# Performance work log

Hardware: AMD Instinct MI355X
Metric: run time of the kernel (lower is better)

## Reference

```python
import jax, jax.numpy as jnp
import numpy as np

B, T, C = 2, 2048, 1024
H = 16
HD = C // H  # head_size = 64
FF = 2 * C   # ffwd_size default = n_embd * 2
EPS = float(jnp.finfo(jnp.float32).eps)  # torch RMSNorm eps=None -> finfo eps


def rmsnorm(x, g):
    # torch.nn.RMSNorm: x / sqrt(mean(x^2) + eps) * weight
    ms = jnp.mean(jnp.square(x), axis=-1, keepdims=True)
    return x * jax.lax.rsqrt(ms + EPS) * g


def setup_inputs() -> dict:
    key = jax.random.key(0)
    ks = jax.random.split(key, 12)
    s_in = 1.0 / np.sqrt(C)
    s_ff = 1.0 / np.sqrt(FF)
    return {
        "target": jax.random.normal(ks[0], (B, T, C), dtype=jnp.float32),
        # per-head projections, torch Linear layout [out, in] stacked over heads: [H, HD, C]
        "wq": jax.random.uniform(ks[1], (H, HD, C), jnp.float32, -s_in, s_in),
        "wk": jax.random.uniform(ks[2], (H, HD, C), jnp.float32, -s_in, s_in),
        "wv": jax.random.uniform(ks[3], (H, HD, C), jnp.float32, -s_in, s_in),
        "w_proj": jax.random.uniform(ks[4], (C, H * HD), jnp.float32, -s_in, s_in),
        "b_proj": jax.random.uniform(ks[5], (C,), jnp.float32, -s_in, s_in),
        "w1": jax.random.uniform(ks[6], (FF, C), jnp.float32, -s_in, s_in),
        "b1": jax.random.uniform(ks[7], (FF,), jnp.float32, -s_in, s_in),
        "w2": jax.random.uniform(ks[8], (C, FF), jnp.float32, -s_ff, s_ff),
        "b2": jax.random.uniform(ks[9], (C,), jnp.float32, -s_ff, s_ff),
        "g1": jnp.ones((C,), jnp.float32),
        "g2": jnp.ones((C,), jnp.float32),
    }


def reference(target, wq, wk, wv, w_proj, b_proj, w1, b1, w2, b2, g1, g2):
    x = rmsnorm(target, g1)
    # q,k,v: [B,H,T,HD]
    q = jnp.einsum("btc,hdc->bhtd", x, wq)
    k = jnp.einsum("btc,hdc->bhtd", x, wk)
    v = jnp.einsum("btc,hdc->bhtd", x, wv)
    scale = HD ** -0.5
    wei = jnp.einsum("bhtd,bhsd->bhts", q, k) * scale  # [B,H,T,T]
    causal = jnp.tril(jnp.ones((T, T), dtype=bool))
    wei = jnp.where(causal, wei, -jnp.inf)
    wei = jax.nn.softmax(wei, axis=-1)
    attn = jnp.einsum("bhts,bhsd->bhtd", wei, v)  # [B,H,T,HD]
    attn = attn.transpose(0, 2, 1, 3).reshape(B, T, H * HD)  # concat heads
    attn = attn @ w_proj.T + b_proj
    target = target + attn
    y = rmsnorm(target, g2)
    h = jax.nn.gelu(y @ w1.T + b1, approximate=False)  # torch nn.GELU default = exact
    ff = h @ w2.T + b2
    return target + ff
```

## Files before the change

### kernel.cpp

```cpp
#include <hip/hip_runtime.h>
#include <math.h>

#define B_  2
#define T_  2048
#define C_  1024
#define H_  16
#define HD_ 64
#define FF_ 2048
#define EPS_ 1.1920929e-07f

typedef __attribute__((ext_vector_type(8))) short short8;
typedef __attribute__((ext_vector_type(4))) float f32x4;

__device__ __forceinline__ unsigned short f2bf(float f) {
    unsigned u = __float_as_uint(f);
    u += 0x7fffu + ((u >> 16) & 1u);
    return (unsigned short)(u >> 16);
}
__device__ __forceinline__ float bf2f(unsigned short u) {
    return __uint_as_float(((unsigned)u) << 16);
}

__global__ void convert_weights(const float* __restrict__ wq, const float* __restrict__ wk,
                                const float* __restrict__ wv, const float* __restrict__ wp,
                                const float* __restrict__ w1, const float* __restrict__ w2,
                                unsigned short* __restrict__ dst) {
    size_t i = ((size_t)blockIdx.x * 256 + threadIdx.x) * 4;
    const float* src; size_t off = i;
    if      (i < 1048576u)  { src = wq; }
    else if (i < 2097152u)  { src = wk; off = i - 1048576u; }
    else if (i < 3145728u)  { src = wv; off = i - 2097152u; }
    else if (i < 4194304u)  { src = wp; off = i - 3145728u; }
    else if (i < 6291456u)  { src = w1; off = i - 4194304u; }
    else                    { src = w2; off = i - 6291456u; }
    float4 v4 = *(const float4*)(src + off);
    ushort4 o4;
    o4.x = f2bf(v4.x); o4.y = f2bf(v4.y); o4.z = f2bf(v4.z); o4.w = f2bf(v4.w);
    *(ushort4*)(dst + i) = o4;
}

__global__ void rmsnorm_bf16_kernel(const float* __restrict__ x, const float* __restrict__ g,
                                    unsigned short* __restrict__ y) {
    int row = blockIdx.x;
    int tid = threadIdx.x;
    const float4* xr = (const float4*)(x + (size_t)row * C_);
    float4 xv = xr[tid];
    float ss = xv.x * xv.x + xv.y * xv.y + xv.z * xv.z + xv.w * xv.w;
    #pragma unroll
    for (int m = 32; m >= 1; m >>= 1) ss += __shfl_xor(ss, m, 64);
    __shared__ float sred[4];
    if ((tid & 63) == 0) sred[tid >> 6] = ss;
    __syncthreads();
    float tot = sred[0] + sred[1] + sred[2] + sred[3];
    float r = rsqrtf(tot * (1.0f / C_) + EPS_);
    float4 gv = ((const float4*)g)[tid];
    ushort4 o;
    o.x = f2bf(xv.x * r * gv.x);
    o.y = f2bf(xv.y * r * gv.y);
    o.z = f2bf(xv.z * r * gv.z);
    o.w = f2bf(xv.w * r * gv.w);
    *((ushort4*)(y + (size_t)row * C_) + tid) = o;
}

template <int ACT, bool BIAS, bool RES, bool OBF16, bool QKV>
__global__ __launch_bounds__(256) void mfma_gemm(
        const unsigned short* __restrict__ A,
        const unsigned short* __restrict__ W0, const unsigned short* __restrict__ W1,
        const unsigned short* __restrict__ W2,
        const float* __restrict__ bias, const float* __restrict__ resid,
        void* __restrict__ O0, void* __restrict__ O1, void* __restrict__ O2,
        int M, int N, int K) {
    __shared__ short As[128 * 32];
    __shared__ short Bs[128 * 32];
    const int tid  = threadIdx.x;
    const int w    = tid >> 6, lane = tid & 63;
    const int tileN = blockIdx.x * 128, tileM = blockIdx.y * 128;

    const unsigned short* Wp = W0;
    void* Op = O0;
    if (QKV) {
        int z = blockIdx.z;
        if (z == 1) { Wp = W1; Op = O1; }
        else if (z == 2) { Wp = W2; Op = O2; }
    }

    const int c0 = 2 * w, c1 = 2 * w + 1;
    const unsigned short* ga0 = A  + (size_t)(tileM + c0 * 16 + (lane >> 2)) * K + (lane & 3) * 8;
    const unsigned short* ga1 = A  + (size_t)(tileM + c1 * 16 + (lane >> 2)) * K + (lane & 3) * 8;
    const unsigned short* gb0 = Wp + (size_t)(tileN + c0 * 16 + (lane >> 2)) * K + (lane & 3) * 8;
    const unsigned short* gb1 = Wp + (size_t)(tileN + c1 * 16 + (lane >> 2)) * K + (lane & 3) * 8;

    f32x4 acc[4][4];
    const f32x4 zed = {0.f, 0.f, 0.f, 0.f};
    #pragma unroll
    for (int i = 0; i < 4; ++i)
        #pragma unroll
        for (int j = 0; j < 4; ++j) acc[i][j] = zed;

    const int wm = (w >> 1) * 64, wn = (w & 1) * 64;
    const int frow = lane & 15, koff = (lane >> 4) * 8;

    for (int k0 = 0; k0 < K; k0 += 32) {
        __builtin_amdgcn_global_load_lds(
            (const __attribute__((address_space(1))) unsigned*)(ga0 + k0),
            (__attribute__((address_space(3))) unsigned*)(As + c0 * 512), 16, 0, 0);
        __builtin_amdgcn_global_load_lds(
            (const __attribute__((address_space(1))) unsigned*)(ga1 + k0),
            (__attribute__((address_space(3))) unsigned*)(As + c1 * 512), 16, 0, 0);
        __builtin_amdgcn_global_load_lds(
            (const __attribute__((address_space(1))) unsigned*)(gb0 + k0),
            (__attribute__((address_space(3))) unsigned*)(Bs + c0 * 512), 16, 0, 0);
        __builtin_amdgcn_global_load_lds(
            (const __attribute__((address_space(1))) unsigned*)(gb1 + k0),
            (__attribute__((address_space(3))) unsigned*)(Bs + c1 * 512), 16, 0, 0);
        __syncthreads();

        short8 af[4], bfr[4];
        #pragma unroll
        for (int i = 0; i < 4; ++i)
            af[i] = *(const short8*)(As + (wm + i * 16 + frow) * 32 + koff);
        #pragma unroll
        for (int j = 0; j < 4; ++j)
            bfr[j] = *(const short8*)(Bs + (wn + j * 16 + frow) * 32 + koff);
        #pragma unroll
        for (int i = 0; i < 4; ++i)
            #pragma unroll
            for (int j = 0; j < 4; ++j)
                acc[i][j] = __builtin_amdgcn_mfma_f32_16x16x32_bf16(af[i], bfr[j], acc[i][j], 0, 0, 0);
        __syncthreads();
    }

    const int ecol = lane & 15, erow = (lane >> 4) * 4;
    const bool isQ  = QKV && (blockIdx.z == 0);
    const bool isVT = QKV && (blockIdx.z == 2);
    #pragma unroll
    for (int j = 0; j < 4; ++j) {
        int n = tileN + wn + j * 16 + ecol;
        float bv = BIAS ? bias[n] : 0.f;
        #pragma unroll
        for (int i = 0; i < 4; ++i) {
            int mbase = tileM + wm + i * 16 + erow;
            #pragma unroll
            for (int r = 0; r < 4; ++r) {
                float val = acc[i][j][r] + bv;
                if (ACT == 1) val = 0.5f * val * (1.0f + erff(val * 0.70710678118654752f));
                int mrow = mbase + r;
                if (isQ) val *= 0.125f;
                if (isVT) {
                    int bb = mrow >> 11, tt = mrow & 2047;
                    int hh = n >> 6, dd = n & 63;
                    size_t idx = ((size_t)((bb * 16 + hh) * 64 + dd)) * 2048 + tt;
                    ((unsigned short*)Op)[idx] = f2bf(val);
                } else {
                    size_t idx = (size_t)mrow * N + n;
                    if (RES) val += resid[idx];
                    if (OBF16) ((unsigned short*)Op)[idx] = f2bf(val);
                    else       ((float*)Op)[idx] = val;
                }
            }
        }
    }
}

__global__ __launch_bounds__(256) void flash_mfma_kernel(
        const unsigned short* __restrict__ q, const unsigned short* __restrict__ k,
        const unsigned short* __restrict__ vT, unsigned short* __restrict__ out) {
    __shared__ unsigned short Ks[64 * 72];
    __shared__ unsigned short Vt[64 * 72];
    __shared__ unsigned short Ps[4 * 16 * 40];

    const int tid  = threadIdx.x;
    const int w    = tid >> 6, lane = tid & 63;
    const int quad = lane >> 4, l15 = lane & 15;
    const int bh = blockIdx.x;
    const int qt = (gridDim.y - 1) - blockIdx.y;
    const int h = bh & (H_ - 1);
    const int b = bh >> 4;

    const size_t qkbase = (size_t)b * T_ * C_ + h * HD_;
    const size_t vbase  = (size_t)(b * H_ + h) * HD_ * T_;

    short8 QB[2];
    {
        const unsigned short* qp = q + qkbase + (size_t)(qt * 64 + w * 16 + l15) * C_;
        QB[0] = *(const short8*)(qp + quad * 8);
        QB[1] = *(const short8*)(qp + 32 + quad * 8);
    }

    f32x4 O[4];
    const f32x4 zed = {0.f, 0.f, 0.f, 0.f};
    #pragma unroll
    for (int dt = 0; dt < 4; ++dt) O[dt] = zed;
    float m_i = -INFINITY, l_i = 0.f;

    const int qg = qt * 64 + w * 16 + l15;
    const int psoff = w * 640 + l15 * 40;
    const int sr = tid >> 3, sp = tid & 7;

    for (int st = 0; st <= qt; ++st) {
        const int s0 = st * 64;
        {
            const unsigned short* kp = k + qkbase + (size_t)(s0 + sr) * C_ + sp * 8;
            *(short8*)&Ks[sr * 72 + sp * 8]        = *(const short8*)kp;
            *(short8*)&Ks[(sr + 32) * 72 + sp * 8] = *(const short8*)(kp + 32 * C_);
            const unsigned short* vp = vT + vbase + (size_t)sr * T_ + s0 + sp * 8;
            *(short8*)&Vt[sr * 72 + sp * 8]        = *(const short8*)vp;
            *(short8*)&Vt[(sr + 32) * 72 + sp * 8] = *(const short8*)(vp + 32 * T_);
        }
        __syncthreads();

        const bool diag = (st == qt);
        #pragma unroll
        for (int sb = 0; sb < 2; ++sb) {
            const int sbl = sb * 32;
            f32x4 Sacc[2];
            #pragma unroll
            for (int u = 0; u < 2; ++u) {
                const unsigned short* kr = &Ks[(sbl + 16 * u + l15) * 72 + quad * 8];
                short8 KA0 = *(const short8*)kr;
                short8 KA1 = *(const short8*)(kr + 32);
                Sacc[u] = __builtin_amdgcn_mfma_f32_16x16x32_bf16(KA0, QB[0], zed, 0, 0, 0);
                Sacc[u] = __builtin_amdgcn_mfma_f32_16x16x32_bf16(KA1, QB[1], Sacc[u], 0, 0, 0);
            }
            float vals[8];
            #pragma unroll
            for (int u = 0; u < 2; ++u)
                #pragma unroll
                for (int r = 0; r < 4; ++r) vals[u * 4 + r] = Sacc[u][r];
            if (diag) {
                #pragma unroll
                for (int u = 0; u < 2; ++u)
                    #pragma unroll
                    for (int r = 0; r < 4; ++r) {
                        int sg = s0 + sbl + 16 * u + quad * 4 + r;
                        if (sg > qg) vals[u * 4 + r] = -INFINITY;
                    }
            }
            float mx = vals[0];
            #pragma unroll
            for (int i = 1; i < 8; ++i) mx = fmaxf(mx, vals[i]);
            mx = fmaxf(mx, __shfl_xor(mx, 16, 64));
            mx = fmaxf(mx, __shfl_xor(mx, 32, 64));
            float mnew = fmaxf(m_i, mx);
            float alpha = __expf(m_i - mnew);
            m_i = mnew;
            float rs = 0.f;
            #pragma unroll
            for (int i = 0; i < 8; ++i) { vals[i] = __expf(vals[i] - mnew); rs += vals[i]; }
            rs += __shfl_xor(rs, 16, 64);
            rs += __shfl_xor(rs, 32, 64);
            l_i = l_i * alpha + rs;

            #pragma unroll
            for (int u = 0; u < 2; ++u) {
                uint2 pw;
                pw.x = (unsigned)f2bf(vals[u * 4 + 0]) | ((unsigned)f2bf(vals[u * 4 + 1]) << 16);
                pw.y = (unsigned)f2bf(vals[u * 4 + 2]) | ((unsigned)f2bf(vals[u * 4 + 3]) << 16);
                *(uint2*)&Ps[psoff + 16 * u + quad * 4] = pw;
            }
            __syncthreads();

            f32x4 av;
            #pragma unroll
            for (int r = 0; r < 4; ++r) av[r] = __shfl(alpha, quad * 4 + r, 64);
            #pragma unroll
            for (int dt = 0; dt < 4; ++dt)
                #pragma unroll
                for (int r = 0; r < 4; ++r) O[dt][r] *= av[r];
            short8 PA = *(const short8*)&Ps[psoff + quad * 8];
            #pragma unroll
            for (int dt = 0; dt < 4; ++dt) {
                short8 VB = *(const short8*)&Vt[(16 * dt + l15) * 72 + sbl + quad * 8];
                O[dt] = __builtin_amdgcn_mfma_f32_16x16x32_bf16(PA, VB, O[dt], 0, 0, 0);
            }
            __syncthreads();
        }
    }

    f32x4 inv;
    #pragma unroll
    for (int r = 0; r < 4; ++r) inv[r] = 1.0f / __shfl(l_i, quad * 4 + r, 64);
    #pragma unroll
    for (int dt = 0; dt < 4; ++dt)
        #pragma unroll
        for (int r = 0; r < 4; ++r) {
            int row = qt * 64 + w * 16 + quad * 4 + r;
            int col = h * HD_ + dt * 16 + l15;
            out[((size_t)(b * T_ + row)) * C_ + col] = f2bf(O[dt][r] * inv[r]);
        }
}

extern "C" void kernel_launch(void* const* d_in, const int* in_sizes, int n_in,
                              void* d_out, int out_size, void* d_ws, size_t ws_size,
                              hipStream_t stream) {
    const float* target = (const float*)d_in[0];
    const float* wq     = (const float*)d_in[1];
    const float* wk     = (const float*)d_in[2];
    const float* wv     = (const float*)d_in[3];
    const float* w_proj = (const float*)d_in[4];
    const float* b_proj = (const float*)d_in[5];
    const float* w1     = (const float*)d_in[6];
    const float* b1     = (const float*)d_in[7];
    const float* w2     = (const float*)d_in[8];
    const float* b2     = (const float*)d_in[9];
    const float* g1     = (const float*)d_in[10];
    const float* g2     = (const float*)d_in[11];
    float* out = (float*)d_out;

    char* ws = (char*)d_ws;
    const size_t MB = 1u << 20;
    unsigned short* xn = (unsigned short*)(ws);
    unsigned short* q  = (unsigned short*)(ws + 8 * MB);
    unsigned short* k  = (unsigned short*)(ws + 16 * MB);
    unsigned short* vt = (unsigned short*)(ws + 24 * MB);
    float*          x2 = (float*)(ws + 32 * MB);
    unsigned short* wb = (unsigned short*)(ws + 48 * MB);
    unsigned short* y  = q;
    unsigned short* hb = k;

    unsigned short* wq_b = wb;
    unsigned short* wk_b = wb + 1048576u;
    unsigned short* wv_b = wb + 2097152u;
    unsigned short* wp_b = wb + 3145728u;
    unsigned short* w1_b = wb + 4194304u;
    unsigned short* w2_b = wb + 6291456u;

    const int M = B_ * T_;

    convert_weights<<<8192, 256, 0, stream>>>(wq, wk, wv, w_proj, w1, w2, wb);
    rmsnorm_bf16_kernel<<<M, 256, 0, stream>>>(target, g1, xn);

    mfma_gemm<0, false, false, true, true><<<dim3(C_ / 128, M / 128, 3), 256, 0, stream>>>(
        xn, wq_b, wk_b, wv_b, nullptr, nullptr, q, k, vt, M, C_, C_);

    flash_mfma_kernel<<<dim3(B_ * H_, T_ / 64), 256, 0, stream>>>(q, k, vt, xn);

    mfma_gemm<0, true, true, false, false><<<dim3(C_ / 128, M / 128, 1), 256, 0, stream>>>(
        xn, wp_b, wp_b, wp_b, b_proj, target, x2, x2, x2, M, C_, C_);

    rmsnorm_bf16_kernel<<<M, 256, 0, stream>>>(x2, g2, y);

    mfma_gemm<1, true, false, true, false><<<dim3(FF_ / 128, M / 128, 1), 256, 0, stream>>>(
        y, w1_b, w1_b, w1_b, b1, nullptr, hb, hb, hb, M, FF_, C_);

    mfma_gemm<0, true, true, false, false><<<dim3(C_ / 128, M / 128, 1), 256, 0, stream>>>(
        hb, w2_b, w2_b, w2_b, b2, x2, out, out, out, M, C_, FF_);
}
```

Before: 338.8 us.

## Templatize GEMM M-tile, fuse QKV into one wide GEMM, double-buffer flash P

The GEMM takes the M tile height as a template parameter and spreads its global-to-LDS chunk loads across warps generically. The proj, FF1 and FF2 GEMMs now use 64-row tiles, which doubles the number of blocks on this large-CU GPU at the cost of less reuse per block. QKV runs as a single N=3072 GEMM that sends each output column to q, k or transposed v by its column range, relying on the three weight matrices sitting next to each other. In the flash kernel the P buffer is double-buffered by sub-block, so the barrier after the PV MFMA moves out of the inner loop, removing one sync per inner iteration at the cost of extra LDS.

```diff
diff --git a/kernel.cpp b/kernel.cpp
--- a/kernel.cpp
+++ b/kernel.cpp
@@ -62,68 +62,63 @@
     *((ushort4*)(y + (size_t)row * C_) + tid) = o;
 }
 
-template <int ACT, bool BIAS, bool RES, bool OBF16, bool QKV>
+template <int TM, int ACT, bool BIAS, bool RES, bool OBF16, int ROUTE>
 __global__ __launch_bounds__(256) void mfma_gemm(
-        const unsigned short* __restrict__ A,
-        const unsigned short* __restrict__ W0, const unsigned short* __restrict__ W1,
-        const unsigned short* __restrict__ W2,
+        const unsigned short* __restrict__ A, const unsigned short* __restrict__ W,
         const float* __restrict__ bias, const float* __restrict__ resid,
         void* __restrict__ O0, void* __restrict__ O1, void* __restrict__ O2,
         int M, int N, int K) {
-    __shared__ short As[128 * 32];
+    constexpr int ACH = TM / 16;
+    constexpr int NCH = (ACH + 8) / 4;
+    constexpr int MI  = TM / 32;
+    __shared__ short As[TM * 32];
     __shared__ short Bs[128 * 32];
     const int tid  = threadIdx.x;
     const int w    = tid >> 6, lane = tid & 63;
-    const int tileN = blockIdx.x * 128, tileM = blockIdx.y * 128;
-
-    const unsigned short* Wp = W0;
-    void* Op = O0;
-    if (QKV) {
-        int z = blockIdx.z;
-        if (z == 1) { Wp = W1; Op = O1; }
-        else if (z == 2) { Wp = W2; Op = O2; }
-    }
-
-    const int c0 = 2 * w, c1 = 2 * w + 1;
-    const unsigned short* ga0 = A  + (size_t)(tileM + c0 * 16 + (lane >> 2)) * K + (lane & 3) * 8;
-    const unsigned short* ga1 = A  + (size_t)(tileM + c1 * 16 + (lane >> 2)) * K + (lane & 3) * 8;
-    const unsigned short* gb0 = Wp + (size_t)(tileN + c0 * 16 + (lane >> 2)) * K + (lane & 3) * 8;
-    const unsigned short* gb1 = Wp + (size_t)(tileN + c1 * 16 + (lane >> 2)) * K + (lane & 3) * 8;
-
-    f32x4 acc[4][4];
+    const int tileN = blockIdx.x * 128, tileM = blockIdx.y * TM;
+
+    const unsigned short* gsrc[NCH];
+    short* ldst[NCH];
+    #pragma unroll
+    for (int i2 = 0; i2 < NCH; ++i2) {
+        int c = w * NCH + i2;
+        if (c < ACH) {
+            gsrc[i2] = A + (size_t)(tileM + c * 16 + (lane >> 2)) * K + (lane & 3) * 8;
+            ldst[i2] = As + c * 512;
+        } else {
+            int c2 = c - ACH;
+            gsrc[i2] = W + (size_t)(tileN + c2 * 16 + (lane >> 2)) * K + (lane & 3) * 8;
+            ldst[i2] = Bs + c2 * 512;
+        }
+    }
+
+    f32x4 acc[MI][4];
     const f32x4 zed = {0.f, 0.f, 0.f, 0.f};
     #pragma unroll
-    for (int i = 0; i < 4; ++i)
+    for (int i = 0; i < MI; ++i)
         #pragma unroll
         for (int j = 0; j < 4; ++j) acc[i][j] = zed;
 
-    const int wm = (w >> 1) * 64, wn = (w & 1) * 64;
+    const int wm = (w >> 1) * (TM / 2), wn = (w & 1) * 64;
     const int frow = lane & 15, koff = (lane >> 4) * 8;
 
     for (int k0 = 0; k0 < K; k0 += 32) {
-        __builtin_amdgcn_global_load_lds(
-            (const __attribute__((address_space(1))) unsigned*)(ga0 + k0),
-            (__attribute__((address_space(3))) unsigned*)(As + c0 * 512), 16, 0, 0);
-        __builtin_amdgcn_global_load_lds(
-            (const __attribute__((address_space(1))) unsigned*)(ga1 + k0),
-            (__attribute__((address_space(3))) unsigned*)(As + c1 * 512), 16, 0, 0);
-        __builtin_amdgcn_global_load_lds(
-            (const __attribute__((address_space(1))) unsigned*)(gb0 + k0),
-            (__attribute__((address_space(3))) unsigned*)(Bs + c0 * 512), 16, 0, 0);
-        __builtin_amdgcn_global_load_lds(
-            (const __attribute__((address_space(1))) unsigned*)(gb1 + k0),
-            (__attribute__((address_space(3))) unsigned*)(Bs + c1 * 512), 16, 0, 0);
+        #pragma unroll
+        for (int i2 = 0; i2 < NCH; ++i2)
+            __builtin_amdgcn_global_load_lds(
+                (const __attribute__((address_space(1))) unsigned*)(gsrc[i2] + k0),
+                (__attribute__((address_space(3))) unsigned*)ldst[i2], 16, 0, 0);
         __syncthreads();
 
-        short8 af[4], bfr[4];
-        #pragma unroll
-        for (int i = 0; i < 4; ++i)
+        short8 af[MI], bfr[4];
+        #pragma unroll
+        for (int i = 0; i < MI; ++i)
             af[i] = *(const short8*)(As + (wm + i * 16 + frow) * 32 + koff);
         #pragma unroll
         for (int j = 0; j < 4; ++j)
             bfr[j] = *(const short8*)(Bs + (wn + j * 16 + frow) * 32 + koff);
         #pragma unroll
-        for (int i = 0; i < 4; ++i)
+        for (int i = 0; i < MI; ++i)
             #pragma unroll
             for (int j = 0; j < 4; ++j)
                 acc[i][j] = __builtin_amdgcn_mfma_f32_16x16x32_bf16(af[i], bfr[j], acc[i][j], 0, 0, 0);
@@ -131,31 +126,35 @@
     }
 
     const int ecol = lane & 15, erow = (lane >> 4) * 4;
-    const bool isQ  = QKV && (blockIdx.z == 0);
-    const bool isVT = QKV && (blockIdx.z == 2);
+    const int zone = ROUTE ? (tileN >> 10) : 0;
     #pragma unroll
     for (int j = 0; j < 4; ++j) {
         int n = tileN + wn + j * 16 + ecol;
         float bv = BIAS ? bias[n] : 0.f;
-        #pragma unroll
-        for (int i = 0; i < 4; ++i) {
+        int nl = ROUTE ? (n & 1023) : n;
+        #pragma unroll
+        for (int i = 0; i < MI; ++i) {
             int mbase = tileM + wm + i * 16 + erow;
             #pragma unroll
             for (int r = 0; r < 4; ++r) {
                 float val = acc[i][j][r] + bv;
                 if (ACT == 1) val = 0.5f * val * (1.0f + erff(val * 0.70710678118654752f));
                 int mrow = mbase + r;
-                if (isQ) val *= 0.125f;
-                if (isVT) {
-                    int bb = mrow >> 11, tt = mrow & 2047;
-                    int hh = n >> 6, dd = n & 63;
-                    size_t idx = ((size_t)((bb * 16 + hh) * 64 + dd)) * 2048 + tt;
-                    ((unsigned short*)Op)[idx] = f2bf(val);
+                if (ROUTE) {
+                    if (zone == 0) {
+                        ((unsigned short*)O0)[(size_t)mrow * 1024 + nl] = f2bf(val * 0.125f);
+                    } else if (zone == 1) {
+                        ((unsigned short*)O1)[(size_t)mrow * 1024 + nl] = f2bf(val);
+                    } else {
+                        int bb = mrow >> 11, tt = mrow & 2047;
+                        int hh = nl >> 6, dd = nl & 63;
+                        ((unsigned short*)O2)[((size_t)((bb * 16 + hh) * 64 + dd)) * 2048 + tt] = f2bf(val);
+                    }
                 } else {
                     size_t idx = (size_t)mrow * N + n;
                     if (RES) val += resid[idx];
-                    if (OBF16) ((unsigned short*)Op)[idx] = f2bf(val);
-                    else       ((float*)Op)[idx] = val;
+                    if (OBF16) ((unsigned short*)O0)[idx] = f2bf(val);
+                    else       ((float*)O0)[idx] = val;
                 }
             }
         }
@@ -167,7 +166,7 @@
         const unsigned short* __restrict__ vT, unsigned short* __restrict__ out) {
     __shared__ unsigned short Ks[64 * 72];
     __shared__ unsigned short Vt[64 * 72];
-    __shared__ unsigned short Ps[4 * 16 * 40];
+    __shared__ unsigned short Ps[2 * 4 * 16 * 40];
 
     const int tid  = threadIdx.x;
     const int w    = tid >> 6, lane = tid & 63;
@@ -256,7 +255,7 @@
                 uint2 pw;
                 pw.x = (unsigned)f2bf(vals[u * 4 + 0]) | ((unsigned)f2bf(vals[u * 4 + 1]) << 16);
                 pw.y = (unsigned)f2bf(vals[u * 4 + 2]) | ((unsigned)f2bf(vals[u * 4 + 3]) << 16);
-                *(uint2*)&Ps[psoff + 16 * u + quad * 4] = pw;
+                *(uint2*)&Ps[sb * 2560 + psoff + 16 * u + quad * 4] = pw;
             }
             __syncthreads();
 
@@ -267,14 +266,14 @@
             for (int dt = 0; dt < 4; ++dt)
                 #pragma unroll
                 for (int r = 0; r < 4; ++r) O[dt][r] *= av[r];
-            short8 PA = *(const short8*)&Ps[psoff + quad * 8];
+            short8 PA = *(const short8*)&Ps[sb * 2560 + psoff + quad * 8];
             #pragma unroll
             for (int dt = 0; dt < 4; ++dt) {
                 short8 VB = *(const short8*)&Vt[(16 * dt + l15) * 72 + sbl + quad * 8];
                 O[dt] = __builtin_amdgcn_mfma_f32_16x16x32_bf16(PA, VB, O[dt], 0, 0, 0);
             }
-            __syncthreads();
-        }
+        }
+        __syncthreads();
     }
 
     f32x4 inv;
@@ -318,31 +317,29 @@
     unsigned short* y  = q;
     unsigned short* hb = k;
 
-    unsigned short* wq_b = wb;
-    unsigned short* wk_b = wb + 1048576u;
-    unsigned short* wv_b = wb + 2097152u;
-    unsigned short* wp_b = wb + 3145728u;
-    unsigned short* w1_b = wb + 4194304u;
-    unsigned short* w2_b = wb + 6291456u;
+    unsigned short* wqkv_b = wb;
+    unsigned short* wp_b   = wb + 3145728u;
+    unsigned short* w1_b   = wb + 4194304u;
+    unsigned short* w2_b   = wb + 6291456u;
 
     const int M = B_ * T_;
 
     convert_weights<<<8192, 256, 0, stream>>>(wq, wk, wv, w_proj, w1, w2, wb);
     rmsnorm_bf16_kernel<<<M, 256, 0, stream>>>(target, g1, xn);
 
-    mfma_gemm<0, false, false, true, true><<<dim3(C_ / 128, M / 128, 3), 256, 0, stream>>>(
-        xn, wq_b, wk_b, wv_b, nullptr, nullptr, q, k, vt, M, C_, C_);
+    mfma_gemm<128, 0, false, false, true, 1><<<dim3(24, M / 128), 256, 0, stream>>>(
+        xn, wqkv_b, nullptr, nullptr, q, k, vt, M, 3072, C_);
 
     flash_mfma_kernel<<<dim3(B_ * H_, T_ / 64), 256, 0, stream>>>(q, k, vt, xn);
 
-    mfma_gemm<0, true, true, false, false><<<dim3(C_ / 128, M / 128, 1), 256, 0, stream>>>(
-        xn, wp_b, wp_b, wp_b, b_proj, target, x2, x2, x2, M, C_, C_);
+    mfma_gemm<64, 0, true, true, false, 0><<<dim3(C_ / 128, M / 64), 256, 0, stream>>>(
+        xn, wp_b, b_proj, target, x2, nullptr, nullptr, M, C_, C_);
 
     rmsnorm_bf16_kernel<<<M, 256, 0, stream>>>(x2, g2, y);
 
-    mfma_gemm<1, true, false, true, false><<<dim3(FF_ / 128, M / 128, 1), 256, 0, stream>>>(
-        y, w1_b, w1_b, w1_b, b1, nullptr, hb, hb, hb, M, FF_, C_);
-
-    mfma_gemm<0, true, true, false, false><<<dim3(C_ / 128, M / 128, 1), 256, 0, stream>>>(
-        hb, w2_b, w2_b, w2_b, b2, x2, out, out, out, M, C_, FF_);
-}
+    mfma_gemm<64, 1, true, false, true, 0><<<dim3(FF_ / 128, M / 64), 256, 0, stream>>>(
+        y, w1_b, b1, nullptr, hb, nullptr, nullptr, M, FF_, C_);
+
+    mfma_gemm<64, 0, true, true, false, 0><<<dim3(C_ / 128, M / 64), 256, 0, stream>>>(
+        hb, w2_b, b2, x2, out, nullptr, nullptr, M, C_, FF_);
+}
```

Measured after the change: 317.8 us. -6.2%, faster.
